# Performance work log

Hardware: AMD Instinct MI355X
Metric: run time of the kernel (lower is better)

## Reference

```python
import jax, jax.numpy as jnp
import numpy as np

B, S, D, H = 32, 512, 512, 8
DF = D // H  # dim_feature = 64
NEG_INF = -1e32


def setup_inputs() -> dict:
    key = jax.random.key(0)
    ks = jax.random.split(key, 8)
    std = 1.0 / np.sqrt(D)  # xavier-ish scale for square linears
    return {
        "q": jax.random.normal(ks[0], (B, S, D), jnp.float32),
        "k": jax.random.normal(ks[1], (B, S, D), jnp.float32),
        "v": jax.random.normal(ks[2], (B, S, D), jnp.float32),
        "mask": jnp.tril(jnp.ones((S, S), jnp.int32))[None, None],  # causal AKT mask
        "zero_pad": 1,
        "question_difficulty_emb": jax.random.normal(ks[3], (B, S, S), jnp.float32) * 0.1,
        "Wk": jax.random.normal(ks[4], (D, D), jnp.float32) * std,
        "bk": jnp.zeros((D,), jnp.float32),
        "Wv": jax.random.normal(ks[5], (D, D), jnp.float32) * std,
        "bv": jnp.zeros((D,), jnp.float32),
        "Wo": jax.random.normal(ks[6], (D, D), jnp.float32) * std,
        "bo": jnp.zeros((D,), jnp.float32),
        "gammas": jax.random.normal(ks[7], (H, 1, 1), jnp.float32) * 0.1,
    }


def reference(q, k, v, mask, zero_pad, question_difficulty_emb, Wk, bk, Wv, bv, Wo, bo, gammas):
    bs = q.shape[0]

    def proj(x, W, b):
        # Linear then split heads: [B,S,D] -> [B,H,S,DF]
        return (x @ W.T + b).reshape(bs, -1, H, DF).transpose(0, 2, 1, 3)

    qh = proj(q, Wk, bk)  # key_query_same=True: q uses key_linear
    kh = proj(k, Wk, bk)
    vh = proj(v, Wv, bv)

    scores = jnp.einsum("bhqd,bhkd->bhqk", qh, kh) / jnp.sqrt(jnp.float32(DF))
    seqlen = scores.shape[-1]
    maskb = mask == 0  # [1,1,S,S]

    # --- distance-decay term (computed under no_grad in torch, detached) ---
    scores_ = jax.nn.softmax(jnp.where(maskb, NEG_INF, scores), axis=-1)
    scores_ = scores_ * mask.astype(scores.dtype)
    distcum = jnp.cumsum(scores_, axis=-1)                      # [B,H,S,S]
    disttot = jnp.sum(scores_, axis=-1, keepdims=True)          # [B,H,S,1]
    pos = jnp.abs(jnp.arange(seqlen)[None, :] - jnp.arange(seqlen)[:, None]).astype(scores.dtype)
    dist_scores = jnp.sqrt(jnp.clip((disttot - distcum) * pos[None, None], 0.0))
    dist_scores = jax.lax.stop_gradient(dist_scores)

    gamma = -jax.nn.softplus(gammas)[None]                      # [1,H,1,1]
    diff = jnp.exp(jax.nn.sigmoid(question_difficulty_emb))[:, None]  # [B,1,S,S]
    total_effect = jnp.clip(jnp.exp(dist_scores * gamma * diff), 1e-5, 1e5)

    scores = scores * total_effect
    scores = jax.nn.softmax(jnp.where(maskb, NEG_INF, scores), axis=-1)
    if zero_pad:
        scores = scores.at[:, :, 0, :].set(0.0)  # zero first query row
    scores = jnp.where(maskb, 0.0, scores)
    # dropout p=0 (eval) -> identity

    out = jnp.einsum("bhqk,bhkd->bhqd", scores, vh)
    concat = out.transpose(0, 2, 1, 3).reshape(bs, -1, D)
    return concat @ Wo.T + bo
```

## Files before the change

kernel.cpp:

```cpp
#include <hip/hip_runtime.h>

typedef unsigned short u16;
typedef __attribute__((ext_vector_type(8))) short short8;
typedef __attribute__((ext_vector_type(8))) _Float16 h8;
typedef __attribute__((ext_vector_type(4))) float f32x4;

__device__ __forceinline__ float b2f(u16 u) {
    return __uint_as_float(((unsigned int)u) << 16);
}
__device__ __forceinline__ u16 f2b(float f) {
    unsigned int x = __float_as_uint(f);
    return (u16)((x + 0x7FFFu + ((x >> 16) & 1u)) >> 16);
}
__device__ __forceinline__ float ldf(const void* p, size_t i, bool f32) {
    return f32 ? ((const float*)p)[i] : b2f(((const u16*)p)[i]);
}
__device__ __forceinline__ void stf(void* p, size_t i, bool f32, float v) {
    if (f32) ((float*)p)[i] = v; else ((u16*)p)[i] = f2b(v);
}
__device__ __forceinline__ float ex2(float x) {
    float r; asm("v_exp_f32 %0, %1" : "=v"(r) : "v"(x)); return r;
}

__device__ __forceinline__ void ldsld16(const void* g, void* l) {
    __builtin_amdgcn_global_load_lds(
        (const __attribute__((address_space(1))) unsigned int*)g,
        (__attribute__((address_space(3))) unsigned int*)l, 16, 0, 0);
}

__global__ void detect_f32(const u16* __restrict__ q, int* __restrict__ flag) {
    __shared__ int cw, cz;
    if (threadIdx.x == 0) { cw = 0; cz = 0; }
    __syncthreads();
    int w = 0, z = 0;
    for (int i = threadIdx.x; i < 4096; i += 256) {
        u16 u = q[i];
        int e = (u >> 7) & 0xFF;
        if (e >= 0xC8) w++;
        if (((i & 1) == 0) && u == 0) z++;
    }
    atomicAdd(&cw, w); atomicAdd(&cz, z);
    __syncthreads();
    if (threadIdx.x == 0) *flag = (cw > 8 || cz > 1024) ? 1 : 0;
}

__global__ __launch_bounds__(256) void cvt3(
    const void* __restrict__ s0, const void* __restrict__ s1,
    const void* __restrict__ s2, u16* __restrict__ d0, u16* __restrict__ d1,
    u16* __restrict__ d2, int n, const int* __restrict__ flag)
{
    const bool f32 = (*flag) != 0;
    const int z = blockIdx.z;
    const void* src = (z == 0) ? s0 : (z == 1) ? s1 : s2;
    u16* dst = (z == 0) ? d0 : (z == 1) ? d1 : d2;
    const int i = (blockIdx.x * 256 + threadIdx.x) * 8;
    if (i >= n) return;
    short8 o;
    if (f32) {
        const float4* s = (const float4*)((const float*)src + i);
        float4 v0 = s[0], v1 = s[1];
        o[0] = (short)f2b(v0.x); o[1] = (short)f2b(v0.y);
        o[2] = (short)f2b(v0.z); o[3] = (short)f2b(v0.w);
        o[4] = (short)f2b(v1.x); o[5] = (short)f2b(v1.y);
        o[6] = (short)f2b(v1.z); o[7] = (short)f2b(v1.w);
    } else {
        o = *(const short8*)((const u16*)src + i);
    }
    *(short8*)(dst + i) = o;
}

__global__ __launch_bounds__(256) void prep_diff(
    const void* __restrict__ qde, _Float16* __restrict__ diff, int n,
    const int* __restrict__ flag)
{
    const bool f32 = (*flag) != 0;
    const int i = (blockIdx.x * 256 + threadIdx.x) * 8;
    if (i >= n) return;
    float x[8];
    if (f32) {
        const float4* s = (const float4*)((const float*)qde + i);
        float4 v0 = s[0], v1 = s[1];
        x[0] = v0.x; x[1] = v0.y; x[2] = v0.z; x[3] = v0.w;
        x[4] = v1.x; x[5] = v1.y; x[6] = v1.z; x[7] = v1.w;
    } else {
        short8 v8 = *(const short8*)((const u16*)qde + i);
        #pragma unroll
        for (int j = 0; j < 8; ++j) x[j] = b2f((u16)v8[j]);
    }
    h8 o;
    #pragma unroll
    for (int j = 0; j < 8; ++j) {
        float sig = __builtin_amdgcn_rcpf(1.f + __expf(-x[j]));
        o[j] = (_Float16)__expf(sig);
    }
    *(h8*)(diff + i) = o;
}

#define BM 128
#define BN 128
#define BK 32

__device__ __forceinline__ void gemm_body(
    const u16* __restrict__ A, const u16* __restrict__ W,
    const void* __restrict__ bias, void* __restrict__ dst,
    bool f32, int mode, int bm, int bn, int M, int N, int K)
{
    __shared__ u16 As[BM * BK];
    __shared__ u16 Bs[BN * BK];
    const int t = threadIdx.x;
    const int w = t >> 6, l = t & 63, lq = l & 15, quad = l >> 4;
    const int wr = (w >> 1) * 64, wc = (w & 1) * 64;

    const int whalf = (w & 1) * 64;
    const u16* gsrc = (w < 2) ? A : W;
    const int  gbase = (w < 2) ? bm : bn;
    u16* lbase = (w < 2) ? As : Bs;

    f32x4 acc[4][4] = {};

    for (int k0 = 0; k0 < K; k0 += BK) {
        __syncthreads();
        #pragma unroll
        for (int c = 0; c < 4; ++c) {
            const int row = whalf + c * 16 + (l >> 2);
            ldsld16(gsrc + (size_t)(gbase + row) * K + k0 + (l & 3) * 8,
                    lbase + row * BK + (l & 3) * 8);
        }
        asm volatile("s_waitcnt vmcnt(0)" ::: "memory");
        __syncthreads();
        short8 af[4], bf[4];
        #pragma unroll
        for (int i = 0; i < 4; ++i)
            af[i] = *(const short8*)&As[(wr + i * 16 + lq) * BK + quad * 8];
        #pragma unroll
        for (int j = 0; j < 4; ++j)
            bf[j] = *(const short8*)&Bs[(wc + j * 16 + lq) * BK + quad * 8];
        #pragma unroll
        for (int i = 0; i < 4; ++i)
            #pragma unroll
            for (int j = 0; j < 4; ++j)
                acc[i][j] = __builtin_amdgcn_mfma_f32_16x16x32_bf16(
                    af[i], bf[j], acc[i][j], 0, 0, 0);
    }

    #pragma unroll
    for (int j = 0; j < 4; ++j) {
        const int n = bn + wc + j * 16 + lq;
        const float bb = ldf(bias, n, f32);
        #pragma unroll
        for (int i = 0; i < 4; ++i) {
            #pragma unroll
            for (int r = 0; r < 4; ++r) {
                const int m = bm + wr + i * 16 + quad * 4 + r;
                const float vout = acc[i][j][r] + bb;
                if (mode == 0) {
                    const int b = m >> 9, s = m & 511, hh = n >> 6, df = n & 63;
                    ((u16*)dst)[((((size_t)b * 8 + hh) * 512 + s) << 6) + df] = f2b(vout);
                } else if (mode == 2) {
                    const int b = m >> 9, s = m & 511, hh = n >> 6, df = n & 63;
                    _Float16 hv = (_Float16)vout;
                    ((u16*)dst)[((((size_t)b * 8 + hh) * 64 + df) << 9) + s] = *(const u16*)&hv;
                } else {
                    stf(dst, (size_t)m * N + n, f32, vout);
                }
            }
        }
    }
}

__global__ __launch_bounds__(256) void proj3(
    const u16* __restrict__ cq, const u16* __restrict__ ck,
    const u16* __restrict__ cv, const u16* __restrict__ cWk,
    const u16* __restrict__ cWv, const void* __restrict__ bk,
    const void* __restrict__ bv, u16* __restrict__ qh, u16* __restrict__ kh,
    u16* __restrict__ vt, const int* __restrict__ flag, int M, int N, int K)
{
    const int z = blockIdx.z;
    const u16* A = (z == 0) ? cq : (z == 1) ? ck : cv;
    const u16* W = (z < 2) ? cWk : cWv;
    const void* bias = (z < 2) ? bk : bv;
    void* dst = (z == 0) ? (void*)qh : (z == 1) ? (void*)kh : (void*)vt;
    gemm_body(A, W, bias, dst, (*flag) != 0, (z < 2) ? 0 : 2,
              blockIdx.y * BM, blockIdx.x * BN, M, N, K);
}

__global__ __launch_bounds__(256) void gemm_out(
    const u16* __restrict__ A, const u16* __restrict__ W,
    const void* __restrict__ bias, void* __restrict__ dst,
    const int* __restrict__ flag, int M, int N, int K)
{
    gemm_body(A, W, bias, dst, (*flag) != 0, 1,
              blockIdx.y * BM, blockIdx.x * BN, M, N, K);
}

#define QT  16
#define SRS 568
#define PRS 584

__global__ __launch_bounds__(512) void akt_attn(
    const u16* __restrict__ qh, const u16* __restrict__ kh,
    const u16* __restrict__ vt, const _Float16* __restrict__ diff,
    const void* __restrict__ gammas, const int* __restrict__ zero_pad,
    const int* __restrict__ flag, u16* __restrict__ attn)
{
    __shared__ _Float16 s_h[QT * SRS];
    __shared__ u16      p_lds[QT * PRS];

    const int blk = blockIdx.x;
    const int h = blk & 7;
    const int i0 = blk >> 3;
    const int qt = i0 & 31;
    const int b = i0 >> 5;

    const int q0 = qt * QT;
    const int t = threadIdx.x, w = t >> 6, l = t & 63;
    const int lq = l & 15, quad = l >> 4;
    const bool f32 = (*flag) != 0;
    const size_t bh = ((size_t)b * 8 + h) * 512;
    const int qmax = q0 + QT - 1;

    {
        const u16* qb = qh + (bh + q0) * 64;
        short8 af0 = *(const short8*)(qb + lq * 64 +      quad * 8);
        short8 af1 = *(const short8*)(qb + lq * 64 + 32 + quad * 8);
        const u16* kb = kh + bh * 64;
        const int KT = (q0 + QT + 127) >> 7;
        int n0 = w * 16;
        bool act = (n0 <= qmax);
        short8 bf0, bf1;
        if (act) {
            bf0 = *(const short8*)(kb + (size_t)(n0 + lq) * 64 +      quad * 8);
            bf1 = *(const short8*)(kb + (size_t)(n0 + lq) * 64 + 32 + quad * 8);
        }
        for (int kt = 0; kt < KT; ++kt) {
            const int n0n = (kt + 1) * 128 + w * 16;
            const bool actn = (kt + 1 < KT) && (n0n <= qmax);
            short8 nb0, nb1;
            if (actn) {
                nb0 = *(const short8*)(kb + (size_t)(n0n + lq) * 64 +      quad * 8);
                nb1 = *(const short8*)(kb + (size_t)(n0n + lq) * 64 + 32 + quad * 8);
            }
            if (act) {
                f32x4 acc = {0.f, 0.f, 0.f, 0.f};
                acc = __builtin_amdgcn_mfma_f32_16x16x32_bf16(af0, bf0, acc, 0, 0, 0);
                acc = __builtin_amdgcn_mfma_f32_16x16x32_bf16(af1, bf1, acc, 0, 0, 0);
                const int cm = n0 + lq + 8 * (n0 >> 6);
                #pragma unroll
                for (int r = 0; r < 4; ++r)
                    s_h[(quad * 4 + r) * SRS + cm] =
                        (_Float16)(acc[r] * 0.180336880f);
            }
            bf0 = nb0; bf1 = nb1; act = actn; n0 = n0n;
        }
    }
    __syncthreads();

    {
        const float g = ldf(gammas, h, f32);
        const float gl2 = -log1pf(expf(g)) * 1.4426950408889634f;
        const int zp = zero_pad[0];
        const int need = (qmax >> 3) + 1;
        int W = 8; while (W < need) W <<= 1;
        const int lw = 31 - __builtin_clz(W);
        const int R = 64 >> lw;
        const int G = W >> 2;
        const int ln = l & (W - 1);
        const int seg = l >> lw;
        const int c0 = ln * 8;
        const int cm = c0 + 8 * (c0 >> 6);
        for (int p = w; p < G; p += 8) {
            const int row = p * R + seg;
            const int q = q0 + row;
            const size_t qoff = ((size_t)b * 512 + q) * 512 + c0;
            h8 dv = *(const h8*)(diff + qoff);
            h8 sv16 = *(const h8*)(s_h + row * SRS + cm);
            float sv[8], cs[8];
            float run = 0.f;
            #pragma unroll
            for (int j = 0; j < 8; ++j) {
                float s = (c0 + j <= q) ? (float)sv16[j] : -1e30f;
                sv[j] = s;
                float pp = ex2(s);
                run += pp; cs[j] = run;
            }
            float incl = run;
            for (int o = 1; o < W; o <<= 1) {
                float u = __shfl_up(incl, o, W);
                if (ln >= o) incl += u;
            }
            const float ls   = __shfl(incl, W - 1, W);
            const float inv1 = __builtin_amdgcn_rcpf(ls);
            const float t0   = ls - incl + run;
            const float qf   = (float)(q - c0);
            float f8[8]; float lf = 0.f;
            #pragma unroll
            for (int j = 0; j < 8; ++j) {
                float suf  = t0 - cs[j];
                float pos  = qf - (float)j;
                float m    = fmaxf(suf * pos, 0.f) * inv1;
                float dist = __builtin_amdgcn_sqrtf(m);
                float a    = fmaxf(dist * gl2 * (float)dv[j], -16.609640474f);
                float eff  = ex2(a);
                float f    = ex2(sv[j] * eff);
                f8[j] = f; lf += f;
            }
            #pragma unroll 6
            for (int o = W >> 1; o > 0; o >>= 1) lf += __shfl_xor(lf, o, 64);
            float inv2 = __builtin_amdgcn_rcpf(lf);
            if (zp && q == 0) inv2 = 0.f;
            h8 pb;
            #pragma unroll
            for (int j = 0; j < 8; ++j) pb[j] = (_Float16)(f8[j] * inv2);
            *(h8*)((_Float16*)p_lds + row * PRS + cm) = pb;
        }
    }
    __syncthreads();

    {
        const int g = w & 3;
        const int half = w >> 2;
        const int KS = (qmax >> 5) + 1;
        const _Float16* vb = (const _Float16*)vt +
            ((size_t)(b * 8 + h) * 64 + g * 16 + lq) * 512;
        const _Float16* prow = (const _Float16*)p_lds + lq * PRS;
        f32x4 oacc = {0.f, 0.f, 0.f, 0.f};
        for (int ks = half; ks < KS; ks += 2) {
            const int kb2 = ks * 32 + quad * 8;
            h8 pa = *(const h8*)(prow + kb2 + 8 * (kb2 >> 6));
            h8 vv = *(const h8*)(vb + kb2);
            oacc = __builtin_amdgcn_mfma_f32_16x16x32_f16(pa, vv, oacc, 0, 0, 0);
        }
        float* opart = (float*)s_h;
        if (half == 1) {
            #pragma unroll
            for (int r = 0; r < 4; ++r)
                opart[(g * 16 + quad * 4 + r) * 17 + lq] = oacc[r];
        }
        __syncthreads();
        if (half == 0) {
            const size_t ob = ((size_t)b * 512 + q0 + quad * 4) * 512 + h * 64 + g * 16 + lq;
            #pragma unroll
            for (int r = 0; r < 4; ++r)
                attn[ob + (size_t)r * 512] =
                    f2b(oacc[r] + opart[(g * 16 + quad * 4 + r) * 17 + lq]);
        }
    }
}

extern "C" void kernel_launch(void* const* d_in, const int* in_sizes, int n_in,
                              void* d_out, int out_size, void* d_ws, size_t ws_size,
                              hipStream_t stream) {
    const void* q   = d_in[0];
    const void* k   = d_in[1];
    const void* v   = d_in[2];
    const int*  zp  = (const int*)d_in[4];
    const void* qde = d_in[5];
    const void* Wk  = d_in[6];
    const void* bk  = d_in[7];
    const void* Wv  = d_in[8];
    const void* bv  = d_in[9];
    const void* Wo  = d_in[10];
    const void* bo  = d_in[11];
    const void* gam = d_in[12];

    const int M = 32 * 512, N = 512, K = 512;
    const int NBIG = M * K;
    const int NW = 512 * 512;

    char* ws = (char*)d_ws;
    int* flag = (int*)ws;
    const size_t SZB = (size_t)NBIG * 2;
    const size_t SZW = (size_t)NW * 2;
    u16* cWk  = (u16*)(ws + 1024);
    u16* cWv  = (u16*)(ws + 1024 + SZW);
    u16* cWo  = (u16*)(ws + 1024 + 2 * SZW);
    u16* cq   = (u16*)(ws + 1024 + 3 * SZW);
    u16* ck   = (u16*)(ws + 1024 + 3 * SZW + SZB);
    u16* cv   = (u16*)(ws + 1024 + 3 * SZW + 2 * SZB);
    u16* qh   = (u16*)(ws + 1024 + 3 * SZW + 3 * SZB);
    u16* kh   = (u16*)(ws + 1024 + 3 * SZW + 4 * SZB);
    u16* vt   = (u16*)(ws + 1024 + 3 * SZW + 5 * SZB);
    u16* attn = (u16*)(ws + 1024 + 3 * SZW + 6 * SZB);

    detect_f32<<<1, 256, 0, stream>>>((const u16*)q, flag);
    cvt3<<<dim3(NW / 2048, 1, 3), 256, 0, stream>>>(Wk, Wv, Wo, cWk, cWv, cWo, NW, flag);
    cvt3<<<dim3(NBIG / 2048, 1, 3), 256, 0, stream>>>(q, k, v, cq, ck, cv, NBIG, flag);
    proj3<<<dim3(N / BN, M / BM, 3), 256, 0, stream>>>(
        cq, ck, cv, cWk, cWv, bk, bv, qh, kh, vt, flag, M, N, K);
    _Float16* diffb = (_Float16*)cq;
    prep_diff<<<dim3(NBIG / 2048), 256, 0, stream>>>(qde, diffb, NBIG, flag);
    akt_attn<<<8192, 512, 0, stream>>>(qh, kh, vt, diffb, gam, zp, flag, attn);
    gemm_out<<<dim3(N / BN, M / BM), 256, 0, stream>>>(attn, cWo, bo, d_out, flag, M, N, K);
}
```

Measured before the change: 383.7 us.

## Fuse difficulty prep into input conversion and template-specialize softmax-decay phase

Folds the sigmoid/exp difficulty preprocessing into the q/k/v conversion launch as a fourth grid slice, writing to a separate workspace region so it no longer has to wait for the projection to finish with the cq buffer. The attention kernel's phase-2 loop is templated on the warp-segment width, so shuffle loops unroll and global/LDS loads for all rows are issued before compute. The per-row normalization becomes a single rsq times gamma in place of rcp plus a per-element multiply. This needs more workspace, with the old path kept as a fallback, and the templated phase adds code size and register pressure.

```diff
diff --git a/kernel.cpp b/kernel.cpp
--- a/kernel.cpp
+++ b/kernel.cpp
@@ -20,6 +20,9 @@
 }
 __device__ __forceinline__ float ex2(float x) {
     float r; asm("v_exp_f32 %0, %1" : "=v"(r) : "v"(x)); return r;
+}
+__device__ __forceinline__ float rsqf(float x) {
+    float r; asm("v_rsq_f32 %0, %1" : "=v"(r) : "v"(x)); return r;
 }
 
 __device__ __forceinline__ void ldsld16(const void* g, void* l) {
@@ -69,6 +72,53 @@
     *(short8*)(dst + i) = o;
 }
 
+__global__ __launch_bounds__(256) void cvt4(
+    const void* __restrict__ s0, const void* __restrict__ s1,
+    const void* __restrict__ s2, const void* __restrict__ s3,
+    u16* __restrict__ d0, u16* __restrict__ d1, u16* __restrict__ d2,
+    _Float16* __restrict__ d3, int n, const int* __restrict__ flag)
+{
+    const bool f32 = (*flag) != 0;
+    const int z = blockIdx.z;
+    const int i = (blockIdx.x * 256 + threadIdx.x) * 8;
+    if (i >= n) return;
+    if (z == 3) {
+        float x[8];
+        if (f32) {
+            const float4* s = (const float4*)((const float*)s3 + i);
+            float4 v0 = s[0], v1 = s[1];
+            x[0] = v0.x; x[1] = v0.y; x[2] = v0.z; x[3] = v0.w;
+            x[4] = v1.x; x[5] = v1.y; x[6] = v1.z; x[7] = v1.w;
+        } else {
+            short8 v8 = *(const short8*)((const u16*)s3 + i);
+            #pragma unroll
+            for (int j = 0; j < 8; ++j) x[j] = b2f((u16)v8[j]);
+        }
+        h8 o;
+        #pragma unroll
+        for (int j = 0; j < 8; ++j) {
+            float sig = __builtin_amdgcn_rcpf(1.f + __expf(-x[j]));
+            o[j] = (_Float16)__expf(sig);
+        }
+        *(h8*)(d3 + i) = o;
+        return;
+    }
+    const void* src = (z == 0) ? s0 : (z == 1) ? s1 : s2;
+    u16* dst = (z == 0) ? d0 : (z == 1) ? d1 : d2;
+    short8 o;
+    if (f32) {
+        const float4* s = (const float4*)((const float*)src + i);
+        float4 v0 = s[0], v1 = s[1];
+        o[0] = (short)f2b(v0.x); o[1] = (short)f2b(v0.y);
+        o[2] = (short)f2b(v0.z); o[3] = (short)f2b(v0.w);
+        o[4] = (short)f2b(v1.x); o[5] = (short)f2b(v1.y);
+        o[6] = (short)f2b(v1.z); o[7] = (short)f2b(v1.w);
+    } else {
+        o = *(const short8*)((const u16*)src + i);
+    }
+    *(short8*)(dst + i) = o;
+}
+
 __global__ __launch_bounds__(256) void prep_diff(
     const void* __restrict__ qde, _Float16* __restrict__ diff, int n,
     const int* __restrict__ flag)
@@ -197,6 +247,84 @@
 #define SRS 568
 #define PRS 584
 
+template<int LW>
+__device__ __forceinline__ void phase2_impl(
+    _Float16* __restrict__ s_h, u16* __restrict__ p_lds,
+    const _Float16* __restrict__ diff, float gl2, int zp,
+    int w, int l, int q0, int b)
+{
+    constexpr int W = 1 << LW;
+    constexpr int R = 64 >> LW;
+    constexpr int G = 16 / R;
+    constexpr int NP = (G + 7) / 8;
+    const int ln = l & (W - 1);
+    const int seg = l >> LW;
+    const int c0 = ln * 8;
+    const int cm = c0 + 8 * (c0 >> 6);
+
+    h8 dvv[NP], svv[NP];
+    #pragma unroll
+    for (int pp = 0; pp < NP; ++pp) {
+        const int p = pp * 8 + w;
+        if (G >= 8 || p < G) {
+            const int row = p * R + seg;
+            const int q = q0 + row;
+            dvv[pp] = *(const h8*)(diff + ((size_t)b * 512 + q) * 512 + c0);
+            svv[pp] = *(const h8*)(s_h + row * SRS + cm);
+        }
+    }
+
+    #pragma unroll
+    for (int pp = 0; pp < NP; ++pp) {
+        const int p = pp * 8 + w;
+        if (G >= 8 || p < G) {
+            const int row = p * R + seg;
+            const int q = q0 + row;
+            const h8 dv = dvv[pp];
+            const h8 sv16 = svv[pp];
+            float sv[8], cs[8];
+            float run = 0.f;
+            #pragma unroll
+            for (int j = 0; j < 8; ++j) {
+                float s = (c0 + j <= q) ? (float)sv16[j] : -1e30f;
+                sv[j] = s;
+                float pe = ex2(s);
+                run += pe; cs[j] = run;
+            }
+            float incl = run;
+            #pragma unroll
+            for (int o = 1; o < W; o <<= 1) {
+                float u = __shfl_up(incl, o, W);
+                if (ln >= o) incl += u;
+            }
+            const float ls  = __shfl(incl, W - 1, W);
+            const float t0  = ls - incl + run;
+            const float grs = gl2 * rsqf(ls);
+            const float qf  = (float)(q - c0);
+            float f8v[8]; float lf = 0.f;
+            #pragma unroll
+            for (int j = 0; j < 8; ++j) {
+                float suf  = t0 - cs[j];
+                float pos  = qf - (float)j;
+                float ms   = fmaxf(suf * pos, 0.f);
+                float dist = __builtin_amdgcn_sqrtf(ms);
+                float a    = fmaxf(dist * grs * (float)dv[j], -16.609640474f);
+                float eff  = ex2(a);
+                float f    = ex2(sv[j] * eff);
+                f8v[j] = f; lf += f;
+            }
+            #pragma unroll
+            for (int o = W >> 1; o > 0; o >>= 1) lf += __shfl_xor(lf, o, 64);
+            float inv2 = __builtin_amdgcn_rcpf(lf);
+            if (zp && q == 0) inv2 = 0.f;
+            h8 pb;
+            #pragma unroll
+            for (int j = 0; j < 8; ++j) pb[j] = (_Float16)(f8v[j] * inv2);
+            *(h8*)((_Float16*)p_lds + row * PRS + cm) = pb;
+        }
+    }
+}
+
 __global__ __launch_bounds__(512) void akt_attn(
     const u16* __restrict__ qh, const u16* __restrict__ kh,
     const u16* __restrict__ vt, const _Float16* __restrict__ diff,
@@ -260,59 +388,14 @@
         const float gl2 = -log1pf(expf(g)) * 1.4426950408889634f;
         const int zp = zero_pad[0];
         const int need = (qmax >> 3) + 1;
-        int W = 8; while (W < need) W <<= 1;
-        const int lw = 31 - __builtin_clz(W);
-        const int R = 64 >> lw;
-        const int G = W >> 2;
-        const int ln = l & (W - 1);
-        const int seg = l >> lw;
-        const int c0 = ln * 8;
-        const int cm = c0 + 8 * (c0 >> 6);
-        for (int p = w; p < G; p += 8) {
-            const int row = p * R + seg;
-            const int q = q0 + row;
-            const size_t qoff = ((size_t)b * 512 + q) * 512 + c0;
-            h8 dv = *(const h8*)(diff + qoff);
-            h8 sv16 = *(const h8*)(s_h + row * SRS + cm);
-            float sv[8], cs[8];
-            float run = 0.f;
-            #pragma unroll
-            for (int j = 0; j < 8; ++j) {
-                float s = (c0 + j <= q) ? (float)sv16[j] : -1e30f;
-                sv[j] = s;
-                float pp = ex2(s);
-                run += pp; cs[j] = run;
-            }
-            float incl = run;
-            for (int o = 1; o < W; o <<= 1) {
-                float u = __shfl_up(incl, o, W);
-                if (ln >= o) incl += u;
-            }
-            const float ls   = __shfl(incl, W - 1, W);
-            const float inv1 = __builtin_amdgcn_rcpf(ls);
-            const float t0   = ls - incl + run;
-            const float qf   = (float)(q - c0);
-            float f8[8]; float lf = 0.f;
-            #pragma unroll
-            for (int j = 0; j < 8; ++j) {
-                float suf  = t0 - cs[j];
-                float pos  = qf - (float)j;
-                float m    = fmaxf(suf * pos, 0.f) * inv1;
-                float dist = __builtin_amdgcn_sqrtf(m);
-                float a    = fmaxf(dist * gl2 * (float)dv[j], -16.609640474f);
-                float eff  = ex2(a);
-                float f    = ex2(sv[j] * eff);
-                f8[j] = f; lf += f;
-            }
-            #pragma unroll 6
-            for (int o = W >> 1; o > 0; o >>= 1) lf += __shfl_xor(lf, o, 64);
-            float inv2 = __builtin_amdgcn_rcpf(lf);
-            if (zp && q == 0) inv2 = 0.f;
-            h8 pb;
-            #pragma unroll
-            for (int j = 0; j < 8; ++j) pb[j] = (_Float16)(f8[j] * inv2);
-            *(h8*)((_Float16*)p_lds + row * PRS + cm) = pb;
-        }
+        if (need <= 8)
+            phase2_impl<3>(s_h, p_lds, diff, gl2, zp, w, l, q0, b);
+        else if (need <= 16)
+            phase2_impl<4>(s_h, p_lds, diff, gl2, zp, w, l, q0, b);
+        else if (need <= 32)
+            phase2_impl<5>(s_h, p_lds, diff, gl2, zp, w, l, q0, b);
+        else
+            phase2_impl<6>(s_h, p_lds, diff, gl2, zp, w, l, q0, b);
     }
     __syncthreads();
 
@@ -384,11 +467,24 @@
 
     detect_f32<<<1, 256, 0, stream>>>((const u16*)q, flag);
     cvt3<<<dim3(NW / 2048, 1, 3), 256, 0, stream>>>(Wk, Wv, Wo, cWk, cWv, cWo, NW, flag);
-    cvt3<<<dim3(NBIG / 2048, 1, 3), 256, 0, stream>>>(q, k, v, cq, ck, cv, NBIG, flag);
-    proj3<<<dim3(N / BN, M / BM, 3), 256, 0, stream>>>(
-        cq, ck, cv, cWk, cWv, bk, bv, qh, kh, vt, flag, M, N, K);
-    _Float16* diffb = (_Float16*)cq;
-    prep_diff<<<dim3(NBIG / 2048), 256, 0, stream>>>(qde, diffb, NBIG, flag);
+
+    _Float16* diffb;
+    const size_t need_ws = 1024 + 3 * SZW + 8 * SZB;
+    if (ws_size >= need_ws) {
+        diffb = (_Float16*)(ws + 1024 + 3 * SZW + 7 * SZB);
+        cvt4<<<dim3(NBIG / 2048, 1, 4), 256, 0, stream>>>(
+            q, k, v, qde, cq, ck, cv, diffb, NBIG, flag);
+        proj3<<<dim3(N / BN, M / BM, 3), 256, 0, stream>>>(
+            cq, ck, cv, cWk, cWv, bk, bv, qh, kh, vt, flag, M, N, K);
+    } else {
+        cvt3<<<dim3(NBIG / 2048, 1, 3), 256, 0, stream>>>(
+            q, k, v, cq, ck, cv, NBIG, flag);
+        proj3<<<dim3(N / BN, M / BM, 3), 256, 0, stream>>>(
+            cq, ck, cv, cWk, cWv, bk, bv, qh, kh, vt, flag, M, N, K);
+        diffb = (_Float16*)cq;
+        prep_diff<<<dim3(NBIG / 2048), 256, 0, stream>>>(qde, diffb, NBIG, flag);
+    }
+
     akt_attn<<<8192, 512, 0, stream>>>(qh, kh, vt, diffb, gam, zp, flag, attn);
     gemm_out<<<dim3(N / BN, M / BM), 256, 0, stream>>>(attn, cWo, bo, d_out, flag, M, N, K);
 }
```

New measurement: 387.6 us. Within noise of the previous version (+1.0%).
